# Optimization experiments

Measured on AMD Instinct MI355X. Metric: run time of the kernel, lower is better.

The kernel has to match this reference:

```python
import jax, jax.numpy as jnp
import numpy as np

NEG_SLOPE = 0.01

def _scatter_mean(vals, idx, num_segments):
    s = jax.ops.segment_sum(vals, idx, num_segments=num_segments)
    cnt = jax.ops.segment_sum(jnp.ones((vals.shape[0],), vals.dtype), idx, num_segments=num_segments)
    return s / jnp.maximum(cnt, 1.0)[:, None]

def setup_inputs() -> dict:
    key = jax.random.key(0)
    ks = jax.random.split(key, 8)
    N, E = 100000, 3200000
    node_emb, edge_emb = 128, 16
    d_in = node_emb + 2 * edge_emb  # 160
    x = jax.random.normal(ks[0], (N, node_emb), dtype=jnp.float32)
    edge_index = jax.random.randint(ks[1], (2, E), 0, N, dtype=jnp.int32)
    edge_attr = jax.random.normal(ks[2], (E, edge_emb), dtype=jnp.float32)
    W1 = jax.random.normal(ks[3], (d_in, node_emb), dtype=jnp.float32) * (1.0 / np.sqrt(d_in))
    b1 = jax.random.normal(ks[4], (node_emb,), dtype=jnp.float32) * 0.01
    W2 = jax.random.normal(ks[5], (node_emb, node_emb), dtype=jnp.float32) * (1.0 / np.sqrt(node_emb))
    b2 = jax.random.normal(ks[6], (node_emb,), dtype=jnp.float32) * 0.01
    return {"x": x, "edge_index": edge_index, "edge_attr": edge_attr,
            "W1": W1, "b1": b1, "W2": W2, "b2": b2}

def reference(x, edge_index, edge_attr, W1, b1, W2, b2):
    N = x.shape[0]
    row, col = edge_index[0], edge_index[1]
    rec_attr = _scatter_mean(edge_attr, row, N)   # [N, edge_emb]
    sent_attr = _scatter_mean(edge_attr, col, N)  # [N, edge_emb]
    out = jnp.concatenate([x, rec_attr, sent_attr], axis=1)  # [N, node+2*edge]
    h = out @ W1 + b1
    h = jnp.where(h >= 0, h, NEG_SLOPE * h)  # LeakyReLU(0.01)
    return h @ W2 + b2
```

## Files before the change

kernel.cpp:

```cpp
#include <hip/hip_runtime.h>
#include <hip/hip_bf16.h>
#include <hip/hip_fp16.h>
#include <stdint.h>

typedef __attribute__((ext_vector_type(8))) short short8;
typedef __attribute__((ext_vector_type(4))) float float4v;

#define NEG_SLOPE 0.01f
#define LDS_S 136

#define FXP_INV_SCALE 0.03125f

#define BSHIFT 8
#define NBMAX 512
#define CHUNK 4096

__device__ __forceinline__ uint16_t f2bf(float f) {
    union { float ff; uint32_t i; } c; c.ff = f;
    uint32_t x = c.i;
    x += 0x7fffu + ((x >> 16) & 1u);
    return (uint16_t)(x >> 16);
}

__device__ __forceinline__ unsigned long long pack4(float4v v) {
    uint32_t u0 = __float2uint_rn(v.x * 32.0f + 256.0f);
    uint32_t u1 = __float2uint_rn(v.y * 32.0f + 256.0f);
    uint32_t u2 = __float2uint_rn(v.z * 32.0f + 256.0f);
    uint32_t u3 = __float2uint_rn(v.w * 32.0f + 256.0f);
    return (unsigned long long)u0
         | ((unsigned long long)u1 << 16)
         | ((unsigned long long)u2 << 32)
         | ((unsigned long long)u3 << 48);
}

__device__ __forceinline__ float4v decode4(unsigned long long pv, float ob, float inv) {
    float4v r;
    r.x = (((float)((uint32_t)(pv       ) & 0xFFFFu)) - ob) * FXP_INV_SCALE * inv;
    r.y = (((float)((uint32_t)(pv >> 16) & 0xFFFFu)) - ob) * FXP_INV_SCALE * inv;
    r.z = (((float)((uint32_t)(pv >> 32) & 0xFFFFu)) - ob) * FXP_INV_SCALE * inv;
    r.w = (((float)((uint32_t)(pv >> 48) & 0xFFFFu)) - ob) * FXP_INV_SCALE * inv;
    return r;
}

__global__ __launch_bounds__(256) void pack_w(
    const float* __restrict__ W1, const float* __restrict__ W2,
    uint16_t* __restrict__ W1p, uint16_t* __restrict__ W2p)
{
    int pid = blockIdx.x * 256 + threadIdx.x;
    if (pid < 20480) {
        int j = pid & 7, lane = (pid >> 3) & 63, rest = pid >> 9;
        int kc = rest % 5, ct = rest / 5;
        int k = kc * 32 + (lane >> 4) * 8 + j;
        int n = ct * 16 + (lane & 15);
        W1p[pid] = f2bf(W1[k * 128 + n]);
    }
    int pid2 = pid - 20480;
    if (pid2 >= 0 && pid2 < 16384) {
        int j = pid2 & 7, lane = (pid2 >> 3) & 63, rest = pid2 >> 9;
        int kc = rest & 3, ct = rest >> 2;
        int k = kc * 32 + (lane >> 4) * 8 + j;
        int n = ct * 16 + (lane & 15);
        W2p[pid2] = f2bf(W2[k * 128 + n]);
    }
}

__global__ __launch_bounds__(256) void hist_kernel(
    const int* __restrict__ eidx, int E,
    uint32_t* __restrict__ cntR, uint32_t* __restrict__ cntC, int NB)
{
    __shared__ uint32_t hR[NBMAX], hC[NBMAX];
    int t = threadIdx.x;
    int cb = blockIdx.x * CHUNK;
    for (int b = t; b < NB; b += 256) { hR[b] = 0; hC[b] = 0; }
    __syncthreads();
    #pragma unroll
    for (int j = 0; j < CHUNK / 256; ++j) {
        int e = cb + t + j * 256;
        if (e < E) {
            atomicAdd(&hR[((uint32_t)eidx[e]) >> BSHIFT], 1u);
            atomicAdd(&hC[((uint32_t)eidx[E + e]) >> BSHIFT], 1u);
        }
    }
    __syncthreads();
    for (int b = t; b < NB; b += 256) {
        if (hR[b]) atomicAdd(cntR + b, hR[b]);
        if (hC[b]) atomicAdd(cntC + b, hC[b]);
    }
}

__global__ __launch_bounds__(256) void scan_kernel(
    const uint32_t* __restrict__ cntR, const uint32_t* __restrict__ cntC,
    uint32_t* __restrict__ baseR, uint32_t* __restrict__ baseC, int NB)
{
    __shared__ uint32_t sR[NBMAX], sC[NBMAX];
    int t = threadIdx.x;
    for (int b = t; b < NB; b += 256) { sR[b] = cntR[b]; sC[b] = cntC[b]; }
    __syncthreads();
    if (t == 0) { uint32_t run = 0; for (int i = 0; i < NB; ++i) { uint32_t u = sR[i]; sR[i] = run; run += u; } }
    if (t == 1) { uint32_t run = 0; for (int i = 0; i < NB; ++i) { uint32_t u = sC[i]; sC[i] = run; run += u; } }
    __syncthreads();
    for (int b = t; b < NB; b += 256) { baseR[b] = sR[b]; baseC[b] = sC[b]; }
}

__global__ __launch_bounds__(256) void binkey_kernel(
    const int* __restrict__ eidx, int E,
    const uint32_t* __restrict__ baseR, const uint32_t* __restrict__ baseC,
    uint32_t* __restrict__ runR, uint32_t* __restrict__ runC,
    uint32_t* __restrict__ keyR, uint32_t* __restrict__ keyC, int NB)
{
    __shared__ uint32_t hR[NBMAX], hC[NBMAX], rkR[NBMAX], rkC[NBMAX];
    __shared__ uint32_t bbR[NBMAX], bbC[NBMAX], gbR[NBMAX], gbC[NBMAX];
    int t = threadIdx.x;
    int cb = blockIdx.x * CHUNK;
    for (int b = t; b < NB; b += 256) {
        hR[b] = 0; hC[b] = 0; rkR[b] = 0; rkC[b] = 0;
        gbR[b] = baseR[b]; gbC[b] = baseC[b];
    }
    __syncthreads();

    uint32_t rows[CHUNK / 256], cols[CHUNK / 256];
    #pragma unroll
    for (int j = 0; j < CHUNK / 256; ++j) {
        int e = cb + t + j * 256;
        if (e < E) {
            rows[j] = (uint32_t)eidx[e];
            cols[j] = (uint32_t)eidx[E + e];
            atomicAdd(&hR[rows[j] >> BSHIFT], 1u);
            atomicAdd(&hC[cols[j] >> BSHIFT], 1u);
        } else rows[j] = 0xFFFFFFFFu;
    }
    __syncthreads();
    for (int b = t; b < NB; b += 256) {
        if (hR[b]) bbR[b] = atomicAdd(runR + b, hR[b]);
        if (hC[b]) bbC[b] = atomicAdd(runC + b, hC[b]);
    }
    __syncthreads();
    #pragma unroll
    for (int j = 0; j < CHUNK / 256; ++j) {
        if (rows[j] != 0xFFFFFFFFu) {
            uint32_t e = (uint32_t)(cb + t + j * 256);
            uint32_t bR = rows[j] >> BSHIFT;
            uint32_t sR = atomicAdd(&rkR[bR], 1u);
            keyR[gbR[bR] + bbR[bR] + sR] = (e << 8) | (rows[j] & 255u);
            uint32_t bC = cols[j] >> BSHIFT;
            uint32_t sC = atomicAdd(&rkC[bC], 1u);
            keyC[gbC[bC] + bbC[bC] + sC] = (e << 8) | (cols[j] & 255u);
        }
    }
}

__global__ __launch_bounds__(256) void reduce_kernel(
    const float* __restrict__ ea,
    const uint32_t* __restrict__ keyR, const uint32_t* __restrict__ keyC,
    const uint32_t* __restrict__ cntR, const uint32_t* __restrict__ cntC,
    const uint32_t* __restrict__ baseR, const uint32_t* __restrict__ baseC,
    float* __restrict__ meanR, float* __restrict__ meanC, int N, int NB)
{
    __shared__ unsigned long long acc[256 * 4];
    __shared__ uint32_t lc[256];
    int blk = blockIdx.x;
    bool isC = blk >= NB;
    int b = isC ? blk - NB : blk;
    const uint32_t* key  = isC ? keyC  : keyR;
    const uint32_t* cnt  = isC ? cntC  : cntR;
    const uint32_t* base = isC ? baseC : baseR;
    float* mean          = isC ? meanC : meanR;

    int t = threadIdx.x;
    for (int i = t; i < 1024; i += 256) acc[i] = 0ull;
    lc[t] = 0;
    __syncthreads();

    uint32_t n = cnt[b];
    uint32_t ba = base[b];
    int part = t & 3, sub = t >> 2;
    for (uint32_t i0 = 0; i0 < n; i0 += 64) {
        uint32_t idx = i0 + sub;
        if (idx < n) {
            uint32_t k = key[ba + idx];
            uint32_t eid = k >> 8;
            uint32_t nl = k & 255u;
            float4v v = ((const float4v*)ea)[(size_t)eid * 4 + part];
            atomicAdd(&acc[nl * 4 + part], pack4(v));
            if (part == 0) atomicAdd(&lc[nl], 1u);
        }
    }
    __syncthreads();

    int node = b * 256 + t;
    if (node < N) {
        uint32_t c = lc[t];
        float inv = c ? 1.0f / (float)c : 0.0f;
        float ob = 256.0f * (float)c;
        #pragma unroll
        for (int j = 0; j < 4; ++j)
            ((float4v*)(mean + (size_t)node * 16))[j] = decode4(acc[t * 4 + j], ob, inv);
    }
}

__global__ __launch_bounds__(256) void scatter_fb(
    const float* __restrict__ ea, const int* __restrict__ idx, int E,
    unsigned long long* __restrict__ pack, uint32_t* __restrict__ fcnt)
{
    int gid = blockIdx.x * 256 + threadIdx.x;
    int e = gid >> 2;
    if (e >= E) return;
    int t = gid & 3;
    float4v v = ((const float4v*)ea)[(size_t)e * 4 + t];
    int n = idx[e];
    atomicAdd(pack + (size_t)n * 4 + t, pack4(v));
    if (t == 0) atomicAdd(fcnt + n, 1u);
}

__global__ __launch_bounds__(256) void finalize_pack(
    const unsigned long long* __restrict__ pack, const uint32_t* __restrict__ fcnt,
    float* __restrict__ mean, int N)
{
    int tid = blockIdx.x * 256 + threadIdx.x;
    if (tid >= N) return;
    uint32_t c = fcnt[tid];
    float inv = c ? 1.0f / (float)c : 0.0f;
    float ob = 256.0f * (float)c;
    #pragma unroll
    for (int j = 0; j < 4; ++j)
        ((float4v*)(mean + (size_t)tid * 16))[j] = decode4(pack[(size_t)tid * 4 + j], ob, inv);
}

__global__ __launch_bounds__(256) void mlp_kernel(
    const float* __restrict__ x,
    const float* __restrict__ meanR, const float* __restrict__ meanC,
    const uint16_t* __restrict__ W1p, const uint16_t* __restrict__ W2p,
    const float* __restrict__ b1, const float* __restrict__ b2,
    float* __restrict__ out, int N)
{
    __shared__ alignas(16) uint16_t hbuf[4 * 16 * LDS_S];
    int wave = threadIdx.x >> 6;
    int lane = threadIdx.x & 63;
    int m = lane & 15, q = lane >> 4;
    int nw = blockIdx.x * 64 + wave * 16;
    int node = nw + m;
    int nclamp = node < N ? node : N - 1;

    short8 afr[5];
    {
        const float* xf = x + (size_t)nclamp * 128;
        #pragma unroll
        for (int kc = 0; kc < 4; ++kc) {
            float4 v0 = *(const float4*)(xf + kc * 32 + q * 8);
            float4 v1 = *(const float4*)(xf + kc * 32 + q * 8 + 4);
            short8 a;
            a[0] = (short)f2bf(v0.x); a[1] = (short)f2bf(v0.y);
            a[2] = (short)f2bf(v0.z); a[3] = (short)f2bf(v0.w);
            a[4] = (short)f2bf(v1.x); a[5] = (short)f2bf(v1.y);
            a[6] = (short)f2bf(v1.z); a[7] = (short)f2bf(v1.w);
            afr[kc] = a;
        }
    }
    {
        const float* msrc = (q < 2) ? (meanR + (size_t)nclamp * 16 + q * 8)
                                    : (meanC + (size_t)nclamp * 16 + (q - 2) * 8);
        float4v v0 = *(const float4v*)msrc;
        float4v v1 = *(const float4v*)(msrc + 4);
        short8 a;
        a[0] = (short)f2bf(v0.x); a[1] = (short)f2bf(v0.y);
        a[2] = (short)f2bf(v0.z); a[3] = (short)f2bf(v0.w);
        a[4] = (short)f2bf(v1.x); a[5] = (short)f2bf(v1.y);
        a[6] = (short)f2bf(v1.z); a[7] = (short)f2bf(v1.w);
        afr[4] = a;
    }

    uint16_t* hw = hbuf + wave * 16 * LDS_S;

    #pragma unroll
    for (int ct = 0; ct < 8; ++ct) {
        float4v acc = {0.f, 0.f, 0.f, 0.f};
        #pragma unroll
        for (int kc = 0; kc < 5; ++kc) {
            short8 bfr = *(const short8*)(W1p + ((ct * 5 + kc) * 64 + lane) * 8);
            acc = __builtin_amdgcn_mfma_f32_16x16x32_bf16(afr[kc], bfr, acc, 0, 0, 0);
        }
        int c = ct * 16 + m;
        float bias = b1[c];
        #pragma unroll
        for (int r = 0; r < 4; ++r) {
            float h = acc[r] + bias;
            h = h >= 0.f ? h : NEG_SLOPE * h;
            hw[(q * 4 + r) * LDS_S + c] = f2bf(h);
        }
    }
    __syncthreads();

    short8 a2[4];
    #pragma unroll
    for (int kc = 0; kc < 4; ++kc)
        a2[kc] = *(const short8*)(hw + m * LDS_S + kc * 32 + q * 8);

    #pragma unroll
    for (int ct = 0; ct < 8; ++ct) {
        float4v acc = {0.f, 0.f, 0.f, 0.f};
        #pragma unroll
        for (int kc = 0; kc < 4; ++kc) {
            short8 bfr = *(const short8*)(W2p + ((ct * 4 + kc) * 64 + lane) * 8);
            acc = __builtin_amdgcn_mfma_f32_16x16x32_bf16(a2[kc], bfr, acc, 0, 0, 0);
        }
        int c = ct * 16 + m;
        float bias = b2[c];
        #pragma unroll
        for (int r = 0; r < 4; ++r) {
            int onode = nw + q * 4 + r;
            if (onode < N)
                out[(size_t)onode * 128 + c] = acc[r] + bias;
        }
    }
}

static inline char* align8(char* p) {
    return (char*)(((uintptr_t)p + 7) & ~(uintptr_t)7);
}

extern "C" void kernel_launch(void* const* d_in, const int* in_sizes, int n_in,
                              void* d_out, int out_size, void* d_ws, size_t ws_size,
                              hipStream_t stream) {
    const float* x   = (const float*)d_in[0];
    const int* eidx  = (const int*)d_in[1];
    const float* ea  = (const float*)d_in[2];
    const float* W1  = (const float*)d_in[3];
    const float* b1  = (const float*)d_in[4];
    const float* W2  = (const float*)d_in[5];
    const float* b2  = (const float*)d_in[6];
    float* out = (float*)d_out;
    int N = in_sizes[0] / 128;
    int E = in_sizes[1] / 2;

    int NB = (N + 255) >> BSHIFT;
    bool fb = (NB > NBMAX) || (E >= (1 << 24));

    float* meanR = (float*)d_ws;
    float* meanC = meanR + (size_t)N * 16;
    uint32_t* keyR = (uint32_t*)(meanC + (size_t)N * 16);
    uint32_t* keyC = keyR + (size_t)E;
    uint32_t* cntR = keyC + (size_t)E;
    uint32_t* cntC = cntR + NB;
    uint32_t* baseR = cntC + NB;
    uint32_t* baseC = baseR + NB;
    uint32_t* runR = baseC + NB;
    uint32_t* runC = runR + NB;
    uint16_t* W1p = (uint16_t*)align8((char*)(runC + NB));
    uint16_t* W2p = W1p + 20480;
    size_t need_main = (size_t)((char*)(W2p + 16384) - (char*)d_ws);
    if (ws_size < need_main) fb = true;

    if (!fb) {
        hipMemsetAsync(cntR, 0, sizeof(uint32_t) * (size_t)NB * 6, stream);
        pack_w<<<(20480 + 16384 + 255) / 256, 256, 0, stream>>>(W1, W2, W1p, W2p);

        int chunks = (E + CHUNK - 1) / CHUNK;
        hist_kernel<<<chunks, 256, 0, stream>>>(eidx, E, cntR, cntC, NB);
        scan_kernel<<<1, 256, 0, stream>>>(cntR, cntC, baseR, baseC, NB);
        binkey_kernel<<<chunks, 256, 0, stream>>>(eidx, E, baseR, baseC,
                                                  runR, runC, keyR, keyC, NB);
        reduce_kernel<<<2 * NB, 256, 0, stream>>>(ea, keyR, keyC, cntR, cntC,
                                                  baseR, baseC, meanR, meanC, N, NB);
    } else {
        float* fmeanR = (float*)d_ws;
        float* fmeanC = fmeanR + (size_t)N * 16;
        unsigned long long* packR = (unsigned long long*)align8((char*)(fmeanC + (size_t)N * 16));
        unsigned long long* packC = packR + (size_t)N * 4;
        uint32_t* fcntR = (uint32_t*)(packC + (size_t)N * 4);
        uint32_t* fcntC = fcntR + N;
        uint16_t* fW1p = (uint16_t*)align8((char*)(fcntC + N));
        uint16_t* fW2p = fW1p + 20480;

        hipMemsetAsync(packR, 0, (size_t)N * 8 * 8 + (size_t)N * 2 * 4, stream);
        pack_w<<<(20480 + 16384 + 255) / 256, 256, 0, stream>>>(W1, W2, fW1p, fW2p);
        int sblocks = (int)(((size_t)E * 4 + 255) / 256);
        scatter_fb<<<sblocks, 256, 0, stream>>>(ea, eidx,     E, packR, fcntR);
        scatter_fb<<<sblocks, 256, 0, stream>>>(ea, eidx + E, E, packC, fcntC);
        int fblocks = (N + 255) / 256;
        finalize_pack<<<fblocks, 256, 0, stream>>>(packR, fcntR, fmeanR, N);
        finalize_pack<<<fblocks, 256, 0, stream>>>(packC, fcntC, fmeanC, N);
        mlp_kernel<<<(N + 63) / 64, 256, 0, stream>>>(x, fmeanR, fmeanC,
                                                      fW1p, fW2p, b1, b2, out, N);
        return;
    }

    mlp_kernel<<<(N + 63) / 64, 256, 0, stream>>>(x, meanR, meanC,
                                                  W1p, W2p, b1, b2, out, N);
}
```

Before: 596.3 us.

## Widen bins, stage binned keys in LDS, split bin reduction across segments

Bins now cover 512 nodes instead of 256, so there are fewer of them. The binning kernel scatters keys into a shared-memory buffer ordered by bin and then copies each bin's run to global memory as a contiguous write, replacing the scattered global stores. The serial scans are replaced by parallel Hillis-Steele scans. The per-bin reduction is split into up to 8 segments per bin, with two loads in flight per iteration; the segment partials go to workspace and a new finalize kernel sums them. This raises parallelism in the reduce step, which had only about 2*NB blocks before, at the cost of extra workspace traffic and an extra launch. The per-bin copy loop in the binning kernel uses one thread per bin writing serially, which may be slow.

```diff
diff --git a/kernel.cpp b/kernel.cpp
--- a/kernel.cpp
+++ b/kernel.cpp
@@ -11,9 +11,11 @@
 
 #define FXP_INV_SCALE 0.03125f
 
-#define BSHIFT 8
-#define NBMAX 512
-#define CHUNK 4096
+#define BSHIFT 9
+#define BMASK 511u
+#define NBMAX 256
+#define CHUNKB 8192
+#define CHUNKH 16384
 
 __device__ __forceinline__ uint16_t f2bf(float f) {
     union { float ff; uint32_t i; } c; c.ff = f;
@@ -70,11 +72,10 @@
 {
     __shared__ uint32_t hR[NBMAX], hC[NBMAX];
     int t = threadIdx.x;
-    int cb = blockIdx.x * CHUNK;
-    for (int b = t; b < NB; b += 256) { hR[b] = 0; hC[b] = 0; }
-    __syncthreads();
-    #pragma unroll
-    for (int j = 0; j < CHUNK / 256; ++j) {
+    int cb = blockIdx.x * CHUNKH;
+    hR[t] = 0; hC[t] = 0;
+    __syncthreads();
+    for (int j = 0; j < CHUNKH / 256; ++j) {
         int e = cb + t + j * 256;
         if (e < E) {
             atomicAdd(&hR[((uint32_t)eidx[e]) >> BSHIFT], 1u);
@@ -82,9 +83,9 @@
         }
     }
     __syncthreads();
-    for (int b = t; b < NB; b += 256) {
-        if (hR[b]) atomicAdd(cntR + b, hR[b]);
-        if (hC[b]) atomicAdd(cntC + b, hC[b]);
+    if (t < NB) {
+        if (hR[t]) atomicAdd(cntR + t, hR[t]);
+        if (hC[t]) atomicAdd(cntC + t, hC[t]);
     }
 }
 
@@ -94,12 +95,18 @@
 {
     __shared__ uint32_t sR[NBMAX], sC[NBMAX];
     int t = threadIdx.x;
-    for (int b = t; b < NB; b += 256) { sR[b] = cntR[b]; sC[b] = cntC[b]; }
-    __syncthreads();
-    if (t == 0) { uint32_t run = 0; for (int i = 0; i < NB; ++i) { uint32_t u = sR[i]; sR[i] = run; run += u; } }
-    if (t == 1) { uint32_t run = 0; for (int i = 0; i < NB; ++i) { uint32_t u = sC[i]; sC[i] = run; run += u; } }
-    __syncthreads();
-    for (int b = t; b < NB; b += 256) { baseR[b] = sR[b]; baseC[b] = sC[b]; }
+    uint32_t vR = (t < NB) ? cntR[t] : 0;
+    uint32_t vC = (t < NB) ? cntC[t] : 0;
+    sR[t] = vR; sC[t] = vC;
+    __syncthreads();
+    for (int off = 1; off < 256; off <<= 1) {
+        uint32_t uR = (t >= off) ? sR[t - off] : 0;
+        uint32_t uC = (t >= off) ? sC[t - off] : 0;
+        __syncthreads();
+        sR[t] += uR; sC[t] += uC;
+        __syncthreads();
+    }
+    if (t < NB) { baseR[t] = sR[t] - vR; baseC[t] = sC[t] - vC; }
 }
 
 __global__ __launch_bounds__(256) void binkey_kernel(
@@ -108,44 +115,62 @@
     uint32_t* __restrict__ runR, uint32_t* __restrict__ runC,
     uint32_t* __restrict__ keyR, uint32_t* __restrict__ keyC, int NB)
 {
-    __shared__ uint32_t hR[NBMAX], hC[NBMAX], rkR[NBMAX], rkC[NBMAX];
-    __shared__ uint32_t bbR[NBMAX], bbC[NBMAX], gbR[NBMAX], gbC[NBMAX];
+    __shared__ uint32_t buf[CHUNKB];
+    __shared__ uint32_t hist[NBMAX], lofs[NBMAX], rk[NBMAX], gb[NBMAX];
     int t = threadIdx.x;
-    int cb = blockIdx.x * CHUNK;
-    for (int b = t; b < NB; b += 256) {
-        hR[b] = 0; hC[b] = 0; rkR[b] = 0; rkC[b] = 0;
-        gbR[b] = baseR[b]; gbC[b] = baseC[b];
-    }
-    __syncthreads();
-
-    uint32_t rows[CHUNK / 256], cols[CHUNK / 256];
-    #pragma unroll
-    for (int j = 0; j < CHUNK / 256; ++j) {
-        int e = cb + t + j * 256;
-        if (e < E) {
-            rows[j] = (uint32_t)eidx[e];
-            cols[j] = (uint32_t)eidx[E + e];
-            atomicAdd(&hR[rows[j] >> BSHIFT], 1u);
-            atomicAdd(&hC[cols[j] >> BSHIFT], 1u);
-        } else rows[j] = 0xFFFFFFFFu;
-    }
-    __syncthreads();
-    for (int b = t; b < NB; b += 256) {
-        if (hR[b]) bbR[b] = atomicAdd(runR + b, hR[b]);
-        if (hC[b]) bbC[b] = atomicAdd(runC + b, hC[b]);
-    }
-    __syncthreads();
-    #pragma unroll
-    for (int j = 0; j < CHUNK / 256; ++j) {
-        if (rows[j] != 0xFFFFFFFFu) {
-            uint32_t e = (uint32_t)(cb + t + j * 256);
-            uint32_t bR = rows[j] >> BSHIFT;
-            uint32_t sR = atomicAdd(&rkR[bR], 1u);
-            keyR[gbR[bR] + bbR[bR] + sR] = (e << 8) | (rows[j] & 255u);
-            uint32_t bC = cols[j] >> BSHIFT;
-            uint32_t sC = atomicAdd(&rkC[bC], 1u);
-            keyC[gbC[bC] + bbC[bC] + sC] = (e << 8) | (cols[j] & 255u);
-        }
+    int cb = blockIdx.x * CHUNKB;
+
+    for (int d = 0; d < 2; ++d) {
+        const int* ids = eidx + (size_t)d * E;
+        uint32_t* runG = d ? runC : runR;
+        const uint32_t* baseG = d ? baseC : baseR;
+        uint32_t* keyG = d ? keyC : keyR;
+
+        hist[t] = 0; rk[t] = 0;
+        __syncthreads();
+
+        uint32_t myid[CHUNKB / 256];
+        #pragma unroll
+        for (int j = 0; j < CHUNKB / 256; ++j) {
+            int i = t + j * 256;
+            if (cb + i < E) {
+                myid[j] = (uint32_t)ids[cb + i];
+                atomicAdd(&hist[myid[j] >> BSHIFT], 1u);
+            } else myid[j] = 0xFFFFFFFFu;
+        }
+        __syncthreads();
+
+        uint32_t v = hist[t];
+        lofs[t] = v;
+        __syncthreads();
+        for (int off = 1; off < 256; off <<= 1) {
+            uint32_t u = (t >= off) ? lofs[t - off] : 0;
+            __syncthreads();
+            lofs[t] += u;
+            __syncthreads();
+        }
+        lofs[t] -= v;
+        if (t < NB && v) gb[t] = atomicAdd(&runG[t], v) + baseG[t];
+        __syncthreads();
+
+        #pragma unroll
+        for (int j = 0; j < CHUNKB / 256; ++j) {
+            if (myid[j] != 0xFFFFFFFFu) {
+                uint32_t b = myid[j] >> BSHIFT;
+                uint32_t p = atomicAdd(&rk[b], 1u);
+                uint32_t e = (uint32_t)(cb + t + j * 256);
+                buf[lofs[b] + p] = (e << BSHIFT) | (myid[j] & BMASK);
+            }
+        }
+        __syncthreads();
+
+        if (t < NB) {
+            uint32_t n = hist[t];
+            uint32_t src = lofs[t];
+            uint32_t dst = gb[t];
+            for (uint32_t i = 0; i < n; ++i) keyG[dst + i] = buf[src + i];
+        }
+        __syncthreads();
     }
 }
 
@@ -154,48 +179,99 @@
     const uint32_t* __restrict__ keyR, const uint32_t* __restrict__ keyC,
     const uint32_t* __restrict__ cntR, const uint32_t* __restrict__ cntC,
     const uint32_t* __restrict__ baseR, const uint32_t* __restrict__ baseC,
-    float* __restrict__ meanR, float* __restrict__ meanC, int N, int NB)
-{
-    __shared__ unsigned long long acc[256 * 4];
-    __shared__ uint32_t lc[256];
+    unsigned long long* __restrict__ pacc, uint32_t* __restrict__ pcnt,
+    float* __restrict__ meanR, float* __restrict__ meanC,
+    int N, int NB, int SEG)
+{
+    __shared__ unsigned long long acc[512 * 4];
+    __shared__ uint32_t lc[512];
     int blk = blockIdx.x;
-    bool isC = blk >= NB;
-    int b = isC ? blk - NB : blk;
-    const uint32_t* key  = isC ? keyC  : keyR;
-    const uint32_t* cnt  = isC ? cntC  : cntR;
-    const uint32_t* base = isC ? baseC : baseR;
-    float* mean          = isC ? meanC : meanR;
+    int dir = blk / (NB * SEG);
+    int rem = blk - dir * NB * SEG;
+    int b = rem / SEG, s = rem - (rem / SEG) * SEG;
+    const uint32_t* key = dir ? keyC : keyR;
+    uint32_t n  = (dir ? cntC  : cntR)[b];
+    uint32_t ba = (dir ? baseC : baseR)[b];
 
     int t = threadIdx.x;
-    for (int i = t; i < 1024; i += 256) acc[i] = 0ull;
-    lc[t] = 0;
-    __syncthreads();
-
-    uint32_t n = cnt[b];
-    uint32_t ba = base[b];
-    int part = t & 3, sub = t >> 2;
-    for (uint32_t i0 = 0; i0 < n; i0 += 64) {
-        uint32_t idx = i0 + sub;
-        if (idx < n) {
-            uint32_t k = key[ba + idx];
-            uint32_t eid = k >> 8;
-            uint32_t nl = k & 255u;
-            float4v v = ((const float4v*)ea)[(size_t)eid * 4 + part];
-            atomicAdd(&acc[nl * 4 + part], pack4(v));
-            if (part == 0) atomicAdd(&lc[nl], 1u);
-        }
-    }
-    __syncthreads();
-
-    int node = b * 256 + t;
-    if (node < N) {
-        uint32_t c = lc[t];
-        float inv = c ? 1.0f / (float)c : 0.0f;
-        float ob = 256.0f * (float)c;
-        #pragma unroll
-        for (int j = 0; j < 4; ++j)
-            ((float4v*)(mean + (size_t)node * 16))[j] = decode4(acc[t * 4 + j], ob, inv);
-    }
+    for (int i = t; i < 2048; i += 256) acc[i] = 0ull;
+    for (int i = t; i < 512; i += 256) lc[i] = 0;
+    __syncthreads();
+
+    uint32_t lo = (uint32_t)(((unsigned long long)n * (unsigned)s) / (unsigned)SEG);
+    uint32_t hi = (uint32_t)(((unsigned long long)n * (unsigned)(s + 1)) / (unsigned)SEG);
+    int p4 = t & 3, sub = t >> 2;
+    for (uint32_t i0 = lo; i0 < hi; i0 += 128) {
+        uint32_t ia = i0 + sub;
+        uint32_t ib = ia + 64;
+        bool va = ia < hi, vb = ib < hi;
+        uint32_t ka = 0, kb = 0;
+        if (va) ka = key[ba + ia];
+        if (vb) kb = key[ba + ib];
+        float4v xa, xb;
+        if (va) xa = ((const float4v*)ea)[(size_t)(ka >> BSHIFT) * 4 + p4];
+        if (vb) xb = ((const float4v*)ea)[(size_t)(kb >> BSHIFT) * 4 + p4];
+        if (va) {
+            atomicAdd(&acc[(ka & BMASK) * 4 + p4], pack4(xa));
+            if (p4 == 0) atomicAdd(&lc[ka & BMASK], 1u);
+        }
+        if (vb) {
+            atomicAdd(&acc[(kb & BMASK) * 4 + p4], pack4(xb));
+            if (p4 == 0) atomicAdd(&lc[kb & BMASK], 1u);
+        }
+    }
+    __syncthreads();
+
+    if (SEG == 1) {
+        float* mean = dir ? meanC : meanR;
+        #pragma unroll
+        for (int u = 0; u < 2; ++u) {
+            int nl = t + u * 256;
+            int node = b * 512 + nl;
+            if (node < N) {
+                uint32_t c = lc[nl];
+                float inv = c ? 1.0f / (float)c : 0.0f;
+                float ob = 256.0f * (float)c;
+                #pragma unroll
+                for (int j = 0; j < 4; ++j)
+                    ((float4v*)(mean + (size_t)node * 16))[j] =
+                        decode4(acc[nl * 4 + j], ob, inv);
+            }
+        }
+    } else {
+        size_t pb = ((size_t)(dir * NB + b) * SEG + s);
+        unsigned long long* pa = pacc + pb * 2048;
+        for (int i = t; i < 2048; i += 256) pa[i] = acc[i];
+        uint32_t* pc = pcnt + pb * 512;
+        for (int i = t; i < 512; i += 256) pc[i] = lc[i];
+    }
+}
+
+__global__ __launch_bounds__(256) void finalize_kernel(
+    const unsigned long long* __restrict__ pacc, const uint32_t* __restrict__ pcnt,
+    float* __restrict__ meanR, float* __restrict__ meanC, int N, int NB, int SEG)
+{
+    int tid = blockIdx.x * 256 + threadIdx.x;
+    if (tid >= 2 * N) return;
+    int dir = tid >= N;
+    int node = dir ? tid - N : tid;
+    int b = node >> BSHIFT, nl = node & (int)BMASK;
+    unsigned long long a0 = 0, a1 = 0, a2 = 0, a3 = 0;
+    uint32_t c = 0;
+    for (int s = 0; s < SEG; ++s) {
+        size_t pb = ((size_t)(dir * NB + b) * SEG + s);
+        const unsigned long long* pa = pacc + pb * 2048 + nl * 4;
+        a0 += pa[0]; a1 += pa[1]; a2 += pa[2]; a3 += pa[3];
+        c += pcnt[pb * 512 + nl];
+    }
+    float inv = c ? 1.0f / (float)c : 0.0f;
+    float ob = 256.0f * (float)c;
+    float* mean = dir ? meanC : meanR;
+    float4v* dst = (float4v*)(mean + (size_t)node * 16);
+    dst[0] = decode4(a0, ob, inv);
+    dst[1] = decode4(a1, ob, inv);
+    dst[2] = decode4(a2, ob, inv);
+    dst[3] = decode4(a3, ob, inv);
 }
 
 __global__ __launch_bounds__(256) void scatter_fb(
@@ -314,8 +390,8 @@
     }
 }
 
-static inline char* align8(char* p) {
-    return (char*)(((uintptr_t)p + 7) & ~(uintptr_t)7);
+static inline char* align16(char* p) {
+    return (char*)(((uintptr_t)p + 15) & ~(uintptr_t)15);
 }
 
 extern "C" void kernel_launch(void* const* d_in, const int* in_sizes, int n_in,
@@ -332,8 +408,8 @@
     int N = in_sizes[0] / 128;
     int E = in_sizes[1] / 2;
 
-    int NB = (N + 255) >> BSHIFT;
-    bool fb = (NB > NBMAX) || (E >= (1 << 24));
+    int NB = (N + 511) >> BSHIFT;
+    bool fb = (NB > NBMAX) || (E >= (1 << 23));
 
     float* meanR = (float*)d_ws;
     float* meanC = meanR + (size_t)N * 16;
@@ -345,30 +421,51 @@
     uint32_t* baseC = baseR + NB;
     uint32_t* runR = baseC + NB;
     uint32_t* runC = runR + NB;
-    uint16_t* W1p = (uint16_t*)align8((char*)(runC + NB));
+    uint16_t* W1p = (uint16_t*)align16((char*)(runC + NB));
     uint16_t* W2p = W1p + 20480;
-    size_t need_main = (size_t)((char*)(W2p + 16384) - (char*)d_ws);
-    if (ws_size < need_main) fb = true;
+    char* pstart = align16((char*)(W2p + 16384));
+    size_t base_need = (size_t)(pstart - (char*)d_ws);
+    int SEG = 0;
+    unsigned long long* pacc = (unsigned long long*)pstart;
+    uint32_t* pcnt = nullptr;
+    if (!fb && ws_size >= base_need) {
+        const int segs[4] = {8, 4, 2, 1};
+        for (int i = 0; i < 4; ++i) {
+            int s = segs[i];
+            size_t pb = (s == 1) ? 0 : (size_t)2 * NB * s * (2048 * 8 + 512 * 4);
+            if (ws_size >= base_need + pb) {
+                SEG = s;
+                pcnt = (uint32_t*)(pstart + (size_t)2 * NB * s * 2048 * 8);
+                break;
+            }
+        }
+    }
+    if (SEG == 0) fb = true;
 
     if (!fb) {
         hipMemsetAsync(cntR, 0, sizeof(uint32_t) * (size_t)NB * 6, stream);
         pack_w<<<(20480 + 16384 + 255) / 256, 256, 0, stream>>>(W1, W2, W1p, W2p);
 
-        int chunks = (E + CHUNK - 1) / CHUNK;
-        hist_kernel<<<chunks, 256, 0, stream>>>(eidx, E, cntR, cntC, NB);
+        hist_kernel<<<(E + CHUNKH - 1) / CHUNKH, 256, 0, stream>>>(eidx, E, cntR, cntC, NB);
         scan_kernel<<<1, 256, 0, stream>>>(cntR, cntC, baseR, baseC, NB);
-        binkey_kernel<<<chunks, 256, 0, stream>>>(eidx, E, baseR, baseC,
-                                                  runR, runC, keyR, keyC, NB);
-        reduce_kernel<<<2 * NB, 256, 0, stream>>>(ea, keyR, keyC, cntR, cntC,
-                                                  baseR, baseC, meanR, meanC, N, NB);
+        binkey_kernel<<<(E + CHUNKB - 1) / CHUNKB, 256, 0, stream>>>(
+            eidx, E, baseR, baseC, runR, runC, keyR, keyC, NB);
+        reduce_kernel<<<2 * NB * SEG, 256, 0, stream>>>(
+            ea, keyR, keyC, cntR, cntC, baseR, baseC,
+            pacc, pcnt, meanR, meanC, N, NB, SEG);
+        if (SEG > 1)
+            finalize_kernel<<<(2 * N + 255) / 256, 256, 0, stream>>>(
+                pacc, pcnt, meanR, meanC, N, NB, SEG);
+        mlp_kernel<<<(N + 63) / 64, 256, 0, stream>>>(x, meanR, meanC,
+                                                      W1p, W2p, b1, b2, out, N);
     } else {
         float* fmeanR = (float*)d_ws;
         float* fmeanC = fmeanR + (size_t)N * 16;
-        unsigned long long* packR = (unsigned long long*)align8((char*)(fmeanC + (size_t)N * 16));
+        unsigned long long* packR = (unsigned long long*)align16((char*)(fmeanC + (size_t)N * 16));
         unsigned long long* packC = packR + (size_t)N * 4;
         uint32_t* fcntR = (uint32_t*)(packC + (size_t)N * 4);
         uint32_t* fcntC = fcntR + N;
-        uint16_t* fW1p = (uint16_t*)align8((char*)(fcntC + N));
+        uint16_t* fW1p = (uint16_t*)align16((char*)(fcntC + N));
         uint16_t* fW2p = fW1p + 20480;
 
         hipMemsetAsync(packR, 0, (size_t)N * 8 * 8 + (size_t)N * 2 * 4, stream);
@@ -381,9 +478,5 @@
         finalize_pack<<<fblocks, 256, 0, stream>>>(packC, fcntC, fmeanC, N);
         mlp_kernel<<<(N + 63) / 64, 256, 0, stream>>>(x, fmeanR, fmeanC,
                                                       fW1p, fW2p, b1, b2, out, N);
-        return;
-    }
-
-    mlp_kernel<<<(N + 63) / 64, 256, 0, stream>>>(x, meanR, meanC,
-                                                  W1p, W2p, b1, b2, out, N);
-}
+    }
+}
```

Result: faster. 554.8 us (-7.0%).
